# Kernel optimization log

Measured on AMD Instinct MI355X. Metric: run time of the kernel, lower is better.

Reference implementation:

```python
import jax, jax.numpy as jnp
import numpy as np

N_NODES = 100000
N_EDGES = 3200000
IN_FEATS = 512
HIDDENS = 256
N_CLASSES = 64
K = 10
ALPHA = 0.1


def setup_inputs() -> dict:
    key = jax.random.key(0)
    k1, k2, k3, k4 = jax.random.split(key, 4)
    features = jax.random.normal(k1, (N_NODES, IN_FEATS), dtype=jnp.float32)
    edge_index = jax.random.randint(k2, (2, N_EDGES), 0, N_NODES, dtype=jnp.int64)
    W1 = jax.random.normal(k3, (IN_FEATS, HIDDENS), dtype=jnp.float32) * (1.0 / np.sqrt(IN_FEATS))
    b1 = jnp.zeros((HIDDENS,), dtype=jnp.float32)
    W2 = jax.random.normal(k4, (HIDDENS, N_CLASSES), dtype=jnp.float32) * (1.0 / np.sqrt(HIDDENS))
    b2 = jnp.zeros((N_CLASSES,), dtype=jnp.float32)
    return {"features": features, "edge_index": edge_index,
            "W1": W1, "b1": b1, "W2": W2, "b2": b2}


def reference(features, edge_index, W1, b1, W2, b2):
    # MLP (dropout=0 -> identity): relu(X W1 + b1) W2 + b2
    h = jax.nn.relu(features @ W1 + b1)      # [N, H]
    h = h @ W2 + b2                          # [N, C]

    src, dst = edge_index[0], edge_index[1]
    ones = jnp.ones((src.shape[0],), dtype=h.dtype)
    out_deg = jax.ops.segment_sum(ones, src, num_segments=N_NODES)
    in_deg = jax.ops.segment_sum(ones, dst, num_segments=N_NODES)
    # symmetric normalization D_out^{-1/2} A D_in^{-1/2}, clamped at 1
    norm_src = jax.lax.rsqrt(jnp.maximum(out_deg, 1.0))
    norm_dst = jax.lax.rsqrt(jnp.maximum(in_deg, 1.0))
    coeff = (norm_src[src] * norm_dst[dst])[:, None]  # [E, 1]

    h0 = h
    for _ in range(K):
        msg = h[src] * coeff                               # gather + scale [E, C]
        agg = jax.ops.segment_sum(msg, dst, num_segments=N_NODES)  # spmm
        h = (1.0 - ALPHA) * agg + ALPHA * h0               # teleport blend
    return h
```

## Files before the change

### kernel.cpp

```cpp
#include <hip/hip_runtime.h>
#include <stdint.h>

#define IN_F 512
#define HID  256
#define CLS  64
#define KPOW 10

typedef unsigned short ushort_t;

typedef __attribute__((ext_vector_type(8))) __bf16    bf16x8;
typedef __attribute__((ext_vector_type(4))) float     f32x4;
typedef __attribute__((ext_vector_type(8))) short     s16x8;
typedef __attribute__((ext_vector_type(8))) _Float16  f16x8;
typedef __attribute__((ext_vector_type(4))) _Float16  f16x4;

__device__ __forceinline__ float b2f(ushort_t u) {
    union { unsigned u; float f; } x; x.u = ((unsigned)u) << 16; return x.f;
}
__device__ __forceinline__ ushort_t f2b(float f) {
    union { float f; unsigned u; } x; x.f = f;
    unsigned u = x.u;
    u += 0x7fffu + ((u >> 16) & 1u);
    return (ushort_t)(u >> 16);
}

__device__ __forceinline__ void gll16(const void* g, void* l) {
    __builtin_amdgcn_global_load_lds(
        (const __attribute__((address_space(1))) unsigned int*)g,
        (__attribute__((address_space(3))) unsigned int*)l, 16, 0, 0);
}

__global__ void k_probe(const ushort_t* __restrict__ feat,
                        const int* __restrict__ eidx,
                        int* __restrict__ flags) {
    if (threadIdx.x == 0 && blockIdx.x == 0) {
        int sane = 0;
        for (int i = 0; i < 128; ++i) {
            unsigned u = (unsigned)feat[2 * i] & 0x7fffu;
            unsigned e = u >> 7;
            if (u == 0u || (e >= 100u && e <= 140u)) sane++;
        }
        flags[0] = (sane == 128) ? 0 : 1;
        int nz = 0;
        for (int i = 0; i < 128; ++i) nz |= eidx[2 * i + 1];
        flags[1] = (nz == 0) ? 1 : 0;
    }
}

__device__ __forceinline__ int edge_at(const int* __restrict__ e, long long i, int wide) {
    return wide ? (int)(((const long long*)e)[i]) : e[i];
}

__global__ void k_degree(const int* __restrict__ eidx, int E,
                         unsigned* __restrict__ oc, unsigned* __restrict__ ic,
                         const int* __restrict__ flags) {
    const int wide = flags[1];
    int e = blockIdx.x * blockDim.x + threadIdx.x;
    if (e < E) {
        atomicAdd(&oc[edge_at(eidx, e, wide)], 1u);
        atomicAdd(&ic[edge_at(eidx, (long long)E + e, wide)], 1u);
    }
}

__global__ void k_norm(const unsigned* __restrict__ oc, const unsigned* __restrict__ ic,
                       float* __restrict__ ns, float* __restrict__ nd9, int N) {
    int i = blockIdx.x * blockDim.x + threadIdx.x;
    if (i < N) {
        ns[i]  = rsqrtf(fmaxf((float)oc[i], 1.0f));
        nd9[i] = 0.9f * rsqrtf(fmaxf((float)ic[i], 1.0f));
    }
}

__global__ void k_scan(const unsigned* __restrict__ cnt, int n,
                       int* __restrict__ offs, int* __restrict__ cursor) {
    __shared__ unsigned ws[16];
    __shared__ unsigned tot;
    const int t    = threadIdx.x;
    const int lane = t & 63;
    const int wid  = t >> 6;
    unsigned carry = 0;
    for (int base = 0; base < n; base += 1024) {
        const int i = base + t;
        const unsigned v = (i < n) ? cnt[i] : 0u;
        unsigned x = v;
        #pragma unroll
        for (int d = 1; d < 64; d <<= 1) {
            unsigned y = __shfl_up(x, d);
            if (lane >= d) x += y;
        }
        if (lane == 63) ws[wid] = x;
        __syncthreads();
        if (wid == 0) {
            const unsigned wv = (lane < 16) ? ws[lane] : 0u;
            unsigned wx = wv;
            #pragma unroll
            for (int d = 1; d < 16; d <<= 1) {
                unsigned y = __shfl_up(wx, d);
                if (lane >= d) wx += y;
            }
            if (lane < 16) ws[lane] = wx - wv;
            if (lane == 15) tot = wx;
        }
        __syncthreads();
        if (i < n) {
            const int o = (int)(carry + ws[wid] + (x - v));
            offs[i]   = o;
            cursor[i] = o;
        }
        carry += tot;
        __syncthreads();
    }
    if (t == 0) offs[n] = (int)carry;
}

__global__ void k_scatter(const int* __restrict__ eidx, int E,
                          int* __restrict__ cursor, int* __restrict__ esrc,
                          const int* __restrict__ flags) {
    const int wide = flags[1];
    int e = blockIdx.x * blockDim.x + threadIdx.x;
    if (e < E) {
        int s = edge_at(eidx, e, wide);
        int d = edge_at(eidx, (long long)E + e, wide);
        int pos = atomicAdd(&cursor[d], 1);
        esrc[pos] = s;
    }
}

__global__ void k_prepw(const void* __restrict__ W1, const void* __restrict__ W2,
                        const void* __restrict__ b1, const void* __restrict__ b2,
                        ushort_t* __restrict__ W1t, ushort_t* __restrict__ W2t,
                        float* __restrict__ bias1, float* __restrict__ bias2,
                        const int* __restrict__ flags) {
    const int f32 = flags[0];
    const int stride = gridDim.x * blockDim.x;
    int t = blockIdx.x * blockDim.x + threadIdx.x;
    for (int i = t; i < IN_F * HID; i += stride) {
        int k = i / HID, n = i % HID;
        float v = f32 ? ((const float*)W1)[i] : b2f(((const ushort_t*)W1)[i]);
        W1t[(size_t)n * IN_F + k] = f2b(v);
    }
    for (int i = t; i < HID * CLS; i += stride) {
        int k = i / CLS, n = i % CLS;
        float v = f32 ? ((const float*)W2)[i] : b2f(((const ushort_t*)W2)[i]);
        W2t[(size_t)n * HID + k] = f2b(v);
    }
    if (t < HID) bias1[t] = f32 ? ((const float*)b1)[t] : b2f(((const ushort_t*)b1)[t]);
    if (t < CLS) bias2[t] = f32 ? ((const float*)b2)[t] : b2f(((const ushort_t*)b2)[t]);
}

template<int BM, int BN, int WM, int WN, int MF, int NF, bool RELU, bool OUT_BF16, bool A_DYN>
__global__ __launch_bounds__(256) void k_gemm_mfma(const void* __restrict__ Xv,
                                                   const ushort_t* __restrict__ Wt,
                                                   const float* __restrict__ biasf,
                                                   void* __restrict__ Cv,
                                                   int M, int K,
                                                   const int* __restrict__ flags) {
    __shared__ ushort_t Ws[BN * 64];
    __shared__ ushort_t Xs[BM * 64];

    const bool xF32 = A_DYN ? (flags[0] != 0) : false;
    const int tid  = threadIdx.x;
    const int lane = tid & 63;
    const int wid  = tid >> 6;
    const int wr   = wid / WN;
    const int wc   = wid % WN;
    const int l15  = lane & 15;
    const int lhi  = lane >> 4;
    const int mbase = blockIdx.x * BM;

    f32x4 acc[MF][NF];
    #pragma unroll
    for (int mf = 0; mf < MF; ++mf)
        #pragma unroll
        for (int nf = 0; nf < NF; ++nf)
            acc[mf][nf] = (f32x4){0.f, 0.f, 0.f, 0.f};

    for (int kt = 0; kt < K; kt += 64) {
        constexpr int CW = (BN * 8) / 256;
        #pragma unroll
        for (int i = 0; i < CW; ++i) {
            const int cid = i * 256 + tid;
            const int n   = cid >> 3;
            const int c   = (cid & 7) ^ (n & 7);
            const ushort_t* src = Wt + (size_t)n * K + kt + c * 8;
            void* dst = (void*)((char*)Ws + (size_t)(i * 256 + wid * 64) * 16);
            gll16((const void*)src, dst);
        }
        constexpr int CX = (BM * 8) / 256;
        #pragma unroll
        for (int i = 0; i < CX; ++i) {
            const int cid = i * 256 + tid;
            const int m   = cid >> 3;
            const int c0  = cid & 7;
            int gr = mbase + m; if (gr >= M) gr = M - 1;
            s16x8 val;
            if (xF32) {
                const float* xp = (const float*)Xv + (size_t)gr * K + kt + c0 * 8;
                const float4 f0 = *(const float4*)(xp);
                const float4 f1 = *(const float4*)(xp + 4);
                val[0] = (short)f2b(f0.x); val[1] = (short)f2b(f0.y);
                val[2] = (short)f2b(f0.z); val[3] = (short)f2b(f0.w);
                val[4] = (short)f2b(f1.x); val[5] = (short)f2b(f1.y);
                val[6] = (short)f2b(f1.z); val[7] = (short)f2b(f1.w);
            } else {
                val = *(const s16x8*)((const ushort_t*)Xv + (size_t)gr * K + kt + c0 * 8);
            }
            *(s16x8*)&Xs[(size_t)(m * 8 + (c0 ^ (m & 7))) * 8] = val;
        }
        __syncthreads();

        #pragma unroll
        for (int ks = 0; ks < 2; ++ks) {
            const int k4 = ks * 4 + lhi;
            bf16x8 wf[NF];
            bf16x8 xf[MF];
            #pragma unroll
            for (int nf = 0; nf < NF; ++nf) {
                const int n = wc * (NF * 16) + nf * 16 + l15;
                wf[nf] = *(const bf16x8*)&Ws[(size_t)(n * 8 + (k4 ^ (n & 7))) * 8];
            }
            #pragma unroll
            for (int mf = 0; mf < MF; ++mf) {
                const int m = wr * (MF * 16) + mf * 16 + l15;
                xf[mf] = *(const bf16x8*)&Xs[(size_t)(m * 8 + (k4 ^ (m & 7))) * 8];
            }
            #pragma unroll
            for (int mf = 0; mf < MF; ++mf)
                #pragma unroll
                for (int nf = 0; nf < NF; ++nf)
                    acc[mf][nf] = __builtin_amdgcn_mfma_f32_16x16x32_bf16(
                        wf[nf], xf[mf], acc[mf][nf], 0, 0, 0);
        }
        __syncthreads();
    }

    #pragma unroll
    for (int nf = 0; nf < NF; ++nf) {
        const int nb = wc * (NF * 16) + nf * 16 + lhi * 4;
        const float4 bb = *(const float4*)&biasf[nb];
        #pragma unroll
        for (int mf = 0; mf < MF; ++mf) {
            const int row = mbase + wr * (MF * 16) + mf * 16 + l15;
            if (row < M) {
                float v0 = acc[mf][nf][0] + bb.x;
                float v1 = acc[mf][nf][1] + bb.y;
                float v2 = acc[mf][nf][2] + bb.z;
                float v3 = acc[mf][nf][3] + bb.w;
                if (RELU) {
                    v0 = fmaxf(v0, 0.f); v1 = fmaxf(v1, 0.f);
                    v2 = fmaxf(v2, 0.f); v3 = fmaxf(v3, 0.f);
                }
                if (OUT_BF16) {
                    ushort4 o;
                    o.x = f2b(v0); o.y = f2b(v1); o.z = f2b(v2); o.w = f2b(v3);
                    *(ushort4*)((ushort_t*)Cv + (size_t)row * BN + nb) = o;
                } else {
                    *(float4*)((float*)Cv + (size_t)row * BN + nb) = make_float4(v0, v1, v2, v3);
                }
            }
        }
    }
}

__global__ void k_init(float* __restrict__ h0a0, _Float16* __restrict__ g0,
                       const float* __restrict__ ns, int total4) {
    int i = blockIdx.x * blockDim.x + threadIdx.x;
    if (i < total4) {
        const int base = i * 4;
        float4 v = *(const float4*)&h0a0[base];
        const float s = ns[base >> 6];
        f16x4 o;
        o[0] = (_Float16)(s * v.x); o[1] = (_Float16)(s * v.y);
        o[2] = (_Float16)(s * v.z); o[3] = (_Float16)(s * v.w);
        *(f16x4*)&g0[base] = o;
        *(float4*)&h0a0[base] = make_float4(0.1f * v.x, 0.1f * v.y, 0.1f * v.z, 0.1f * v.w);
    }
}

template<bool LAST>
__global__ __launch_bounds__(256) void k_prop(const _Float16* __restrict__ g,
                                              const float* __restrict__ a0,
                                              const int* __restrict__ esrc,
                                              const int* __restrict__ offs,
                                              const float* __restrict__ nd9,
                                              const float* __restrict__ ns,
                                              void* __restrict__ out, int N) {
    const int lane = threadIdx.x & 63;
    const int wid  = threadIdx.x >> 6;
    const int v    = blockIdx.x * 4 + wid;
    if (v >= N) return;

    const int sub = lane >> 3;
    const int q8  = (lane & 7) << 3;
    const int start = offs[v];
    const int end   = offs[v + 1];

    float accA[8] = {0.f,0.f,0.f,0.f,0.f,0.f,0.f,0.f};
    float accB[8] = {0.f,0.f,0.f,0.f,0.f,0.f,0.f,0.f};

    int i = start;
    for (; i + 16 <= end; i += 16) {
        const int s0 = esrc[i + sub];
        const int s1 = esrc[i + 8 + sub];
        const f16x8 r0 = *(const f16x8*)&g[(size_t)s0 * CLS + q8];
        const f16x8 r1 = *(const f16x8*)&g[(size_t)s1 * CLS + q8];
        #pragma unroll
        for (int j = 0; j < 8; ++j) { accA[j] += (float)r0[j]; accB[j] += (float)r1[j]; }
    }
    if (i + 8 <= end) {
        const int s0 = esrc[i + sub];
        const f16x8 r0 = *(const f16x8*)&g[(size_t)s0 * CLS + q8];
        #pragma unroll
        for (int j = 0; j < 8; ++j) accA[j] += (float)r0[j];
        i += 8;
    }
    if (i < end && sub < end - i) {
        const int s0 = esrc[i + sub];
        const f16x8 r0 = *(const f16x8*)&g[(size_t)s0 * CLS + q8];
        #pragma unroll
        for (int j = 0; j < 8; ++j) accB[j] += (float)r0[j];
    }

    float r[8];
    #pragma unroll
    for (int j = 0; j < 8; ++j) {
        float x = accA[j] + accB[j];
        x += __shfl_xor(x, 8);
        x += __shfl_xor(x, 16);
        x += __shfl_xor(x, 32);
        r[j] = x;
    }

    if (sub == 0) {
        const size_t idx = (size_t)v * CLS + q8;
        const float c = nd9[v];
        const float4 t0 = *(const float4*)&a0[idx];
        const float4 t1 = *(const float4*)&a0[idx + 4];
        float h0 = fmaf(c, r[0], t0.x);
        float h1 = fmaf(c, r[1], t0.y);
        float h2 = fmaf(c, r[2], t0.z);
        float h3 = fmaf(c, r[3], t0.w);
        float h4 = fmaf(c, r[4], t1.x);
        float h5 = fmaf(c, r[5], t1.y);
        float h6 = fmaf(c, r[6], t1.z);
        float h7 = fmaf(c, r[7], t1.w);
        if (LAST) {
            float* po = (float*)out + idx;
            *(float4*)(po)     = make_float4(h0, h1, h2, h3);
            *(float4*)(po + 4) = make_float4(h4, h5, h6, h7);
        } else {
            const float s = ns[v];
            f16x8 o;
            o[0] = (_Float16)(s * h0); o[1] = (_Float16)(s * h1);
            o[2] = (_Float16)(s * h2); o[3] = (_Float16)(s * h3);
            o[4] = (_Float16)(s * h4); o[5] = (_Float16)(s * h5);
            o[6] = (_Float16)(s * h6); o[7] = (_Float16)(s * h7);
            *(f16x8*)((_Float16*)out + idx) = o;
        }
    }
}

extern "C" void kernel_launch(void* const* d_in, const int* in_sizes, int n_in,
                              void* d_out, int out_size, void* d_ws, size_t ws_size,
                              hipStream_t stream) {
    const ushort_t* feat = (const ushort_t*)d_in[0];
    const int*      eidx = (const int*)d_in[1];
    const void*     W1   = d_in[2];
    const void*     b1   = d_in[3];
    const void*     W2   = d_in[4];
    const void*     b2   = d_in[5];

    const int N = in_sizes[0] / IN_F;
    const int E = in_sizes[1] / 2;

    char* w = (char*)d_ws;
    auto take = [&](size_t bytes) -> char* {
        char* p = w; w += (bytes + 255) & ~(size_t)255; return p;
    };
    int*      flags = (int*)take(256);
    unsigned* oc    = (unsigned*)take((size_t)N * 4);
    unsigned* ic    = (unsigned*)take((size_t)N * 4);
    float*    ns    = (float*)take((size_t)N * 4);
    float*    nd9   = (float*)take((size_t)N * 4);
    int*      offs  = (int*)take((size_t)(N + 1) * 4);
    int*      curs  = (int*)take((size_t)N * 4);
    int*      esrc  = (int*)take((size_t)E * 4);
    ushort_t* W1t   = (ushort_t*)take((size_t)HID * IN_F * 2);
    ushort_t* W2t   = (ushort_t*)take((size_t)CLS * HID * 2);
    float*    bias1 = (float*)take((size_t)HID * 4);
    float*    bias2 = (float*)take((size_t)CLS * 4);
    float*    h0a0  = (float*)take((size_t)N * CLS * 4);
    char*     regG  = take((size_t)N * HID * 2);
    ushort_t* H1 = (ushort_t*)regG;
    _Float16* gA = (_Float16*)regG;
    _Float16* gB = (_Float16*)(regG + (size_t)N * CLS * 2);

    hipMemsetAsync(oc, 0, (size_t)N * 4, stream);
    hipMemsetAsync(ic, 0, (size_t)N * 4, stream);

    k_probe<<<1, 64, 0, stream>>>(feat, eidx, flags);
    k_prepw<<<256, 256, 0, stream>>>(W1, W2, b1, b2, W1t, W2t, bias1, bias2, flags);

    const int gE = (E + 255) / 256;
    k_degree<<<gE, 256, 0, stream>>>(eidx, E, oc, ic, flags);
    k_norm<<<(N + 255) / 256, 256, 0, stream>>>(oc, ic, ns, nd9, N);
    k_scan<<<1, 1024, 0, stream>>>(ic, N, offs, curs);
    k_scatter<<<gE, 256, 0, stream>>>(eidx, E, curs, esrc, flags);

    k_gemm_mfma<64, 256, 1, 4, 4, 4, true, true, true>
        <<<(N + 63) / 64, 256, 0, stream>>>(feat, W1t, bias1, (void*)H1, N, IN_F, flags);
    k_gemm_mfma<128, 64, 2, 2, 4, 2, false, false, false>
        <<<(N + 127) / 128, 256, 0, stream>>>(H1, W2t, bias2, (void*)h0a0, N, HID, flags);

    const int total4 = (N * CLS) / 4;
    k_init<<<(total4 + 255) / 256, 256, 0, stream>>>(h0a0, gA, ns, total4);

    const int gp = (N + 3) / 4;
    for (int it = 0; it < KPOW; ++it) {
        const _Float16* gin = (it & 1) ? gB : gA;
        if (it == KPOW - 1) {
            k_prop<true ><<<gp, 256, 0, stream>>>(gin, h0a0, esrc, offs, nd9, ns, d_out, N);
        } else {
            _Float16* gout = (it & 1) ? gA : gB;
            k_prop<false><<<gp, 256, 0, stream>>>(gin, h0a0, esrc, offs, nd9, ns, (void*)gout, N);
        }
    }
}
```

Measured before the change: 1.571 ms.

## Pack edges to int32 and bucket CSR scatter into destination-range passes

The degree kernel now also writes compacted int32 src/dst arrays, reusing the h0a0 buffer when it is large enough. The CSR scatter becomes a multi-pass kernel: each pass reads all edges with vector loads but only inserts those whose destination falls in one of eight node ranges, keeping cursor atomics and esrc writes localized for cache reuse. The propagation kernel is also unrolled to four independent gathers per iteration to keep more loads in flight. The cost is reading the edge list eight times during the scatter, plus extra register pressure in the propagation kernel.

Measured after the change: 1.529 ms. -2.7%, faster.

```diff
diff --git a/kernel.cpp b/kernel.cpp
--- a/kernel.cpp
+++ b/kernel.cpp
@@ -5,6 +5,7 @@
 #define HID  256
 #define CLS  64
 #define KPOW 10
+#define NPASS 8
 
 typedef unsigned short ushort_t;
 
@@ -51,14 +52,19 @@
     return wide ? (int)(((const long long*)e)[i]) : e[i];
 }
 
-__global__ void k_degree(const int* __restrict__ eidx, int E,
-                         unsigned* __restrict__ oc, unsigned* __restrict__ ic,
-                         const int* __restrict__ flags) {
+__global__ void k_pack(const int* __restrict__ eidx, int E,
+                       int* __restrict__ es32, int* __restrict__ ed32,
+                       unsigned* __restrict__ oc, unsigned* __restrict__ ic,
+                       const int* __restrict__ flags) {
     const int wide = flags[1];
     int e = blockIdx.x * blockDim.x + threadIdx.x;
     if (e < E) {
-        atomicAdd(&oc[edge_at(eidx, e, wide)], 1u);
-        atomicAdd(&ic[edge_at(eidx, (long long)E + e, wide)], 1u);
+        const int s = edge_at(eidx, e, wide);
+        const int d = edge_at(eidx, (long long)E + e, wide);
+        es32[e] = s;
+        ed32[e] = d;
+        atomicAdd(&oc[s], 1u);
+        atomicAdd(&ic[d], 1u);
     }
 }
 
@@ -113,16 +119,29 @@
     if (t == 0) offs[n] = (int)carry;
 }
 
-__global__ void k_scatter(const int* __restrict__ eidx, int E,
-                          int* __restrict__ cursor, int* __restrict__ esrc,
-                          const int* __restrict__ flags) {
-    const int wide = flags[1];
-    int e = blockIdx.x * blockDim.x + threadIdx.x;
-    if (e < E) {
-        int s = edge_at(eidx, e, wide);
-        int d = edge_at(eidx, (long long)E + e, wide);
-        int pos = atomicAdd(&cursor[d], 1);
-        esrc[pos] = s;
+__global__ __launch_bounds__(256) void k_scatter_mp(const int* __restrict__ es32,
+                                                    const int* __restrict__ ed32,
+                                                    int E, int* __restrict__ cursor,
+                                                    int* __restrict__ esrc,
+                                                    int range, int bpp) {
+    const int pass = blockIdx.x / bpp;
+    const int b    = blockIdx.x % bpp;
+    const int lo   = pass * range;
+    const int hi   = lo + range;
+
+    const int stride = bpp * 256 * 4;
+    for (int e = (b * 256 + threadIdx.x) * 4; e + 3 < E; e += stride) {
+        const int4 d = *(const int4*)&ed32[e];
+        const int4 s = *(const int4*)&es32[e];
+        if (d.x >= lo && d.x < hi) esrc[atomicAdd(&cursor[d.x], 1)] = s.x;
+        if (d.y >= lo && d.y < hi) esrc[atomicAdd(&cursor[d.y], 1)] = s.y;
+        if (d.z >= lo && d.z < hi) esrc[atomicAdd(&cursor[d.z], 1)] = s.z;
+        if (d.w >= lo && d.w < hi) esrc[atomicAdd(&cursor[d.w], 1)] = s.w;
+    }
+    if (blockIdx.x == gridDim.x - 1 && threadIdx.x < (E & 3)) {
+        const int e = (E & ~3) + threadIdx.x;
+        const int d = ed32[e];
+        esrc[atomicAdd(&cursor[d], 1)] = es32[e];
     }
 }
 
@@ -295,36 +314,54 @@
     const int start = offs[v];
     const int end   = offs[v + 1];
 
-    float accA[8] = {0.f,0.f,0.f,0.f,0.f,0.f,0.f,0.f};
-    float accB[8] = {0.f,0.f,0.f,0.f,0.f,0.f,0.f,0.f};
+    float aA[8] = {0.f,0.f,0.f,0.f,0.f,0.f,0.f,0.f};
+    float aB[8] = {0.f,0.f,0.f,0.f,0.f,0.f,0.f,0.f};
+    float aC[8] = {0.f,0.f,0.f,0.f,0.f,0.f,0.f,0.f};
+    float aD[8] = {0.f,0.f,0.f,0.f,0.f,0.f,0.f,0.f};
 
     int i = start;
-    for (; i + 16 <= end; i += 16) {
+    for (; i + 32 <= end; i += 32) {
+        const int s0 = esrc[i + sub];
+        const int s1 = esrc[i + 8  + sub];
+        const int s2 = esrc[i + 16 + sub];
+        const int s3 = esrc[i + 24 + sub];
+        const f16x8 r0 = *(const f16x8*)&g[(size_t)s0 * CLS + q8];
+        const f16x8 r1 = *(const f16x8*)&g[(size_t)s1 * CLS + q8];
+        const f16x8 r2 = *(const f16x8*)&g[(size_t)s2 * CLS + q8];
+        const f16x8 r3 = *(const f16x8*)&g[(size_t)s3 * CLS + q8];
+        #pragma unroll
+        for (int j = 0; j < 8; ++j) {
+            aA[j] += (float)r0[j]; aB[j] += (float)r1[j];
+            aC[j] += (float)r2[j]; aD[j] += (float)r3[j];
+        }
+    }
+    if (i + 16 <= end) {
         const int s0 = esrc[i + sub];
         const int s1 = esrc[i + 8 + sub];
         const f16x8 r0 = *(const f16x8*)&g[(size_t)s0 * CLS + q8];
         const f16x8 r1 = *(const f16x8*)&g[(size_t)s1 * CLS + q8];
         #pragma unroll
-        for (int j = 0; j < 8; ++j) { accA[j] += (float)r0[j]; accB[j] += (float)r1[j]; }
+        for (int j = 0; j < 8; ++j) { aA[j] += (float)r0[j]; aB[j] += (float)r1[j]; }
+        i += 16;
     }
     if (i + 8 <= end) {
         const int s0 = esrc[i + sub];
         const f16x8 r0 = *(const f16x8*)&g[(size_t)s0 * CLS + q8];
         #pragma unroll
-        for (int j = 0; j < 8; ++j) accA[j] += (float)r0[j];
+        for (int j = 0; j < 8; ++j) aC[j] += (float)r0[j];
         i += 8;
     }
     if (i < end && sub < end - i) {
         const int s0 = esrc[i + sub];
         const f16x8 r0 = *(const f16x8*)&g[(size_t)s0 * CLS + q8];
         #pragma unroll
-        for (int j = 0; j < 8; ++j) accB[j] += (float)r0[j];
+        for (int j = 0; j < 8; ++j) aD[j] += (float)r0[j];
     }
 
     float r[8];
     #pragma unroll
     for (int j = 0; j < 8; ++j) {
-        float x = accA[j] + accB[j];
+        float x = (aA[j] + aB[j]) + (aC[j] + aD[j]);
         x += __shfl_xor(x, 8);
         x += __shfl_xor(x, 16);
         x += __shfl_xor(x, 32);
@@ -395,6 +432,11 @@
     _Float16* gA = (_Float16*)regG;
     _Float16* gB = (_Float16*)(regG + (size_t)N * CLS * 2);
 
+    int* es32;
+    if ((size_t)E * 8 <= (size_t)N * CLS * 4) es32 = (int*)h0a0;
+    else                                      es32 = (int*)take((size_t)E * 8);
+    int* ed32 = es32 + E;
+
     hipMemsetAsync(oc, 0, (size_t)N * 4, stream);
     hipMemsetAsync(ic, 0, (size_t)N * 4, stream);
 
@@ -402,10 +444,13 @@
     k_prepw<<<256, 256, 0, stream>>>(W1, W2, b1, b2, W1t, W2t, bias1, bias2, flags);
 
     const int gE = (E + 255) / 256;
-    k_degree<<<gE, 256, 0, stream>>>(eidx, E, oc, ic, flags);
+    k_pack<<<gE, 256, 0, stream>>>(eidx, E, es32, ed32, oc, ic, flags);
     k_norm<<<(N + 255) / 256, 256, 0, stream>>>(oc, ic, ns, nd9, N);
     k_scan<<<1, 1024, 0, stream>>>(ic, N, offs, curs);
-    k_scatter<<<gE, 256, 0, stream>>>(eidx, E, curs, esrc, flags);
+
+    const int range = (N + NPASS - 1) / NPASS;
+    const int bpp   = 800;
+    k_scatter_mp<<<NPASS * bpp, 256, 0, stream>>>(es32, ed32, E, curs, esrc, range, bpp);
 
     k_gemm_mfma<64, 256, 1, 4, 4, 4, true, true, true>
         <<<(N + 63) / 64, 256, 0, stream>>>(feat, W1t, bias1, (void*)H1, N, IN_F, flags);
```
